# Optimization experiments

Measured on AMD Instinct MI355X. Metric: run time of the kernel, lower is better.

## Reference

```python
import jax, jax.numpy as jnp
import numpy as np

B, N, F, IMF = 16, 64, 512, 2048
EPS = 1e-5


def _linear_params(key, out_f, in_f):
    k1, k2 = jax.random.split(key)
    w = jax.random.normal(k1, (out_f, in_f), dtype=jnp.float32) * 0.02
    b = jax.random.normal(k2, (out_f,), dtype=jnp.float32) * 0.02
    return w, b


def setup_inputs() -> dict:
    key = jax.random.key(0)
    ks = jax.random.split(key, 8)
    inp = {}
    inp["input"] = jax.random.normal(ks[0], (B, N, F), dtype=jnp.float32)
    inp["im_input"] = jax.random.normal(ks[1], (B, IMF), dtype=jnp.float32)
    inp["gmlp1_w"], inp["gmlp1_b"] = _linear_params(ks[2], F, 2 * F)
    inp["gmlp2_w"], inp["gmlp2_b"] = _linear_params(ks[3], F, F)
    inp["gmlp3_w"], inp["gmlp3_b"] = _linear_params(ks[4], F, F)
    inp["im_w"], inp["im_b"] = _linear_params(ks[5], F, IMF)
    inp["bn_gamma"] = jnp.ones((F,), dtype=jnp.float32)
    inp["bn_beta"] = jnp.zeros((F,), dtype=jnp.float32)
    inp["d1_w"], inp["d1_b"] = _linear_params(ks[6], F, 2 * F)
    inp["d2_w"], inp["d2_b"] = _linear_params(ks[7], 2, F)
    return inp


def reference(input, im_input, gmlp1_w, gmlp1_b, gmlp2_w, gmlp2_b,
              gmlp3_w, gmlp3_b, im_w, im_b, bn_gamma, bn_beta,
              d1_w, d1_b, d2_w, d2_b):
    b, n, f = input.shape
    npair = n * n
    # relation_embedding: all-pairs expand + concat (replicating the exact
    # row-major reshape semantics of the original torch code, including the
    # memory-reinterpreting view used for feature2)
    feature1 = jnp.broadcast_to(input[:, None, :, :], (b, n, n, f)).reshape(b, npair, f)
    feature2 = jnp.broadcast_to(input[:, :, :, None], (b, n, f, n)).reshape(b, npair, f)
    feature = jnp.concatenate([feature1, feature2], axis=2).reshape(-1, 2 * f)  # [b*n^2, 1024]
    h = jax.nn.relu(feature @ gmlp1_w.T + gmlp1_b)
    h = jax.nn.relu(h @ gmlp2_w.T + gmlp2_b)
    h = jax.nn.relu(h @ gmlp3_w.T + gmlp3_b)
    sent_embedding = h.reshape(b, npair, f).mean(axis=1)  # [b, 512]
    # im_embedding: Linear + BatchNorm1d (training-mode batch stats) + ReLU
    img = im_input @ im_w.T + im_b
    mu = img.mean(axis=0)
    var = jnp.mean(jnp.square(img - mu), axis=0)  # biased variance
    img = bn_gamma * (img - mu) * jax.lax.rsqrt(var + EPS) + bn_beta
    img_embedding = jax.nn.relu(img)
    # net_D
    emb = jnp.concatenate([sent_embedding, img_embedding], axis=1)  # [b, 1024]
    out = jax.nn.relu(emb @ d1_w.T + d1_b) @ d2_w.T + d2_b  # [b, 2]
    return out
```

## Files before the change

kernel.cpp:

```cpp
#include <hip/hip_runtime.h>


typedef float f32x4 __attribute__((ext_vector_type(4)));
typedef __bf16 bf16x8v __attribute__((ext_vector_type(8)));
typedef __bf16 bf16x4v __attribute__((ext_vector_type(4)));

#define WS_A1Q     0u
#define WS_W1P     2097152u
#define WS_SENT    2129920u
#define WS_Y       2162688u
#define WS_IMGEMB  2195456u
#define WS_W2BF    2228224u
#define WS_W3BF    2752512u

__global__ __launch_bounds__(256) void k_prep(
    const float* __restrict__ input, const float* __restrict__ im_input,
    const float* __restrict__ g1w, const float* __restrict__ g1b,
    const float* __restrict__ g2w, const float* __restrict__ g3w,
    const float* __restrict__ imw, const float* __restrict__ imb,
    float* __restrict__ ws)
{
  __shared__ float As[16][72];
  __shared__ float Bs[16][72];
  const int blk = blockIdx.x, t = threadIdx.x;
  float4* A1Q = (float4*)ws;
  __bf16* w1p = (__bf16*)((char*)ws + WS_W1P);
  float* sent = (float*)((char*)ws + WS_SENT);
  float* yv   = (float*)((char*)ws + WS_Y);
  __bf16* w2bf = (__bf16*)((char*)ws + WS_W2BF);
  __bf16* w3bf = (__bf16*)((char*)ws + WS_W3BF);

  if (blk < 128) {
    const int tm = blk >> 3, tn = blk & 7;
    const int m0 = tm * 64, o0 = tn * 64;
    const int ty = t >> 4, tx = t & 15;
    const int lrow = t >> 2, lk4 = (t & 3) * 4;
    float acc[4][4] = {};
    for (int kc = 0; kc < 512; kc += 16) {
      float4 av = *(const float4*)(input + (m0 + lrow) * 512 + kc + lk4);
      float4 bw = *(const float4*)(g1w + (size_t)(o0 + lrow) * 1024 + kc + lk4);
      __syncthreads();
      As[lk4 + 0][lrow] = av.x; As[lk4 + 1][lrow] = av.y;
      As[lk4 + 2][lrow] = av.z; As[lk4 + 3][lrow] = av.w;
      Bs[lk4 + 0][lrow] = bw.x; Bs[lk4 + 1][lrow] = bw.y;
      Bs[lk4 + 2][lrow] = bw.z; Bs[lk4 + 3][lrow] = bw.w;
      __syncthreads();
#pragma unroll
      for (int kk = 0; kk < 16; ++kk) {
        float a4[4], b4[4];
        *(float4*)a4 = *(const float4*)&As[kk][4 * ty];
        *(float4*)b4 = *(const float4*)&Bs[kk][4 * tx];
#pragma unroll
        for (int ii = 0; ii < 4; ++ii)
#pragma unroll
          for (int jj = 0; jj < 4; ++jj)
            acc[ii][jj] += a4[ii] * b4[jj];
      }
    }
    float4 bias = *(const float4*)(g1b + o0 + 4 * tx);
#pragma unroll
    for (int ii = 0; ii < 4; ++ii) {
      float4 v;
      v.x = acc[ii][0] + bias.x; v.y = acc[ii][1] + bias.y;
      v.z = acc[ii][2] + bias.z; v.w = acc[ii][3] + bias.w;
      A1Q[(tm * 128 + tn * 16 + tx) * 64 + 4 * ty + ii] = v;
    }
  } else if (blk < 384) {
    int idx = ((blk - 128) * 256 + t) * 8;
    const float* src; __bf16* dst; int off;
    if (idx < 262144) { src = g2w; dst = w2bf; off = idx; }
    else              { src = g3w; dst = w3bf; off = idx - 262144; }
    int o = off >> 9, k = off & 511;
    int ks = k >> 5, quad = (k >> 3) & 3;
    int doff = (o >> 4) * 8192 + ks * 512 + (quad * 16 + (o & 15)) * 8;
    float4 v0 = *(const float4*)(src + off);
    float4 v1 = *(const float4*)(src + off + 4);
    bf16x8v h;
    h[0] = (__bf16)v0.x; h[1] = (__bf16)v0.y; h[2] = (__bf16)v0.z; h[3] = (__bf16)v0.w;
    h[4] = (__bf16)v1.x; h[5] = (__bf16)v1.y; h[6] = (__bf16)v1.z; h[7] = (__bf16)v1.w;
    *(bf16x8v*)(dst + doff) = h;
  } else if (blk < 400) {
    int idx = (blk - 384) * 256 + t;
    int o = idx >> 3, s = idx & 7;
    const float* p = g1w + (size_t)o * 1024 + 512 + s * 64;
    float sum = 0.f;
#pragma unroll
    for (int u = 0; u < 64; u += 4) {
      float4 v = *(const float4*)(p + u);
      sum += v.x + v.y + v.z + v.w;
    }
    int base = (o >> 4) * 512 + (o & 15) * 8 + s;
    w1p[base]       = (__bf16)sum;
    w1p[base + 128] = (__bf16)0.f;
    w1p[base + 256] = (__bf16)0.f;
    w1p[base + 384] = (__bf16)0.f;
    sent[idx] = 0.f; sent[idx + 4096] = 0.f;
  } else {
    int o = blk - 400;
    int wv = t >> 6, l = t & 63;
    const float* wrow = imw + (size_t)o * 2048;
    for (int bb = 0; bb < 4; ++bb) {
      int b = wv * 4 + bb;
      const float* xr = im_input + (size_t)b * 2048;
      float s = 0.f;
#pragma unroll
      for (int u = 0; u < 8; ++u) {
        int k = u * 256 + l * 4;
        float4 xv = *(const float4*)(xr + k);
        float4 wx = *(const float4*)(wrow + k);
        s += xv.x * wx.x + xv.y * wx.y + xv.z * wx.z + xv.w * wx.w;
      }
#pragma unroll
      for (int m = 32; m >= 1; m >>= 1) s += __shfl_xor(s, m);
      if (l == 0) yv[b * 512 + o] = s + imb[o];
    }
  }
}

__device__ __forceinline__ void kloop(const __bf16* __restrict__ wl,
                                      const __bf16* __restrict__ hbuf,
                                      int p16, int quad, f32x4 acc[4][8])
{
  const int msk3 = (p16 & 7) << 3;
  int moff[8];
#pragma unroll
  for (int mt = 0; mt < 8; ++mt)
    moff[mt] = (mt >> 2) * 32768 + (p16 + 16 * (mt & 3)) * 512;
  bf16x8v a[4], an[4];
#pragma unroll
  for (int ot = 0; ot < 4; ++ot) a[ot] = *(const bf16x8v*)(wl + ot * 8192);
#pragma unroll 2
  for (int ks = 0; ks < 16; ++ks) {
    const int kcb = (((ks * 4 + quad) << 3) ^ msk3);
    bf16x8v bf[8];
#pragma unroll
    for (int mt = 0; mt < 8; ++mt)
      bf[mt] = *(const bf16x8v*)(hbuf + moff[mt] + kcb);
    if (ks < 15) {
#pragma unroll
      for (int ot = 0; ot < 4; ++ot)
        an[ot] = *(const bf16x8v*)(wl + (ks + 1) * 512 + ot * 8192);
    }
#pragma unroll
    for (int ot = 0; ot < 4; ++ot)
#pragma unroll
      for (int mt = 0; mt < 4; ++mt)
        acc[ot][mt] = __builtin_amdgcn_mfma_f32_16x16x32_bf16(a[ot], bf[mt], acc[ot][mt], 0, 0, 0);
#pragma unroll
    for (int ot = 0; ot < 4; ++ot)
#pragma unroll
      for (int mt = 4; mt < 8; ++mt)
        acc[ot][mt] = __builtin_amdgcn_mfma_f32_16x16x32_bf16(a[ot], bf[mt], acc[ot][mt], 0, 0, 0);
    if (ks < 15) {
#pragma unroll
      for (int ot = 0; ot < 4; ++ot) a[ot] = an[ot];
    }
  }
}

__global__ __launch_bounds__(512, 2) void k_main(
    const float* __restrict__ input,
    const float* __restrict__ g2b, const float* __restrict__ g3b,
    const float* __restrict__ bng, const float* __restrict__ bnb,
    float* __restrict__ ws)
{
  const int blk = blockIdx.x, t = threadIdx.x;
  const float4* A1Q = (const float4*)ws;
  const __bf16* w1p = (const __bf16*)((char*)ws + WS_W1P);
  float* sent = (float*)((char*)ws + WS_SENT);
  float* yv   = (float*)((char*)ws + WS_Y);
  float* imge = (float*)((char*)ws + WS_IMGEMB);
  const __bf16* w2bf = (const __bf16*)((char*)ws + WS_W2BF);
  const __bf16* w3bf = (const __bf16*)((char*)ws + WS_W3BF);

  if (blk == 512) {
    int o = t;
    float vals[16];
    float mu = 0.f;
#pragma unroll
    for (int b = 0; b < 16; ++b) { vals[b] = yv[b * 512 + o]; mu += vals[b]; }
    mu *= (1.f / 16.f);
    float var = 0.f;
#pragma unroll
    for (int b = 0; b < 16; ++b) { float d = vals[b] - mu; var += d * d; }
    var *= (1.f / 16.f);
    float sc = bng[o] * rsqrtf(var + 1e-5f);
    float sh = bnb[o] - mu * sc;
#pragma unroll
    for (int b = 0; b < 16; ++b)
      imge[b * 512 + o] = fmaxf(vals[b] * sc + sh, 0.f);
    return;
  }

  __shared__ __align__(16) __bf16 hbuf[65536];

  const int b = blk >> 5, ipair = blk & 31;
  const int w = t >> 6, l = t & 63;
  const int quad = l >> 4, p16 = l & 15;

  float xreg0[8], xreg1[8];
  {
    const float* xr0 = input + (size_t)(b * 64 + ipair * 2) * 512 + l * 8;
    *(float4*)xreg0       = *(const float4*)xr0;
    *(float4*)(xreg0 + 4) = *(const float4*)(xr0 + 4);
    *(float4*)xreg1       = *(const float4*)(xr0 + 512);
    *(float4*)(xreg1 + 4) = *(const float4*)(xr0 + 516);
  }

  f32x4 acc[4][8];

  {
    bf16x8v xb[8];
#pragma unroll
    for (int mt = 0; mt < 4; ++mt) {
#pragma unroll
      for (int j = 0; j < 8; ++j) {
        float v0 = __shfl(xreg0[j], p16 + 16 * mt);
        float v1 = __shfl(xreg1[j], p16 + 16 * mt);
        xb[mt][j]     = (quad == 0) ? (__bf16)v0 : (__bf16)0.f;
        xb[mt + 4][j] = (quad == 0) ? (__bf16)v1 : (__bf16)0.f;
      }
    }
#pragma unroll
    for (int ot = 0; ot < 4; ++ot)
#pragma unroll
      for (int mt = 0; mt < 8; ++mt) { f32x4 z = {0.f, 0.f, 0.f, 0.f}; acc[ot][mt] = z; }
#pragma unroll
    for (int ot = 0; ot < 4; ++ot) {
      bf16x8v af = *(const bf16x8v*)(w1p + (w * 4 + ot) * 512 + l * 8);
#pragma unroll
      for (int mt = 0; mt < 8; ++mt)
        acc[ot][mt] = __builtin_amdgcn_mfma_f32_16x16x32_bf16(af, xb[mt], acc[ot][mt], 0, 0, 0);
    }
    const float4* cq = A1Q + ((size_t)b * 128 + w * 16) * 64;
#pragma unroll
    for (int ot = 0; ot < 4; ++ot) {
#pragma unroll
      for (int mtp = 0; mtp < 4; ++mtp) {
        float4 c = cq[(ot * 4 + quad) * 64 + 16 * mtp + p16];
        int row = p16 + 16 * mtp;
        int col = w * 64 + ot * 16 + quad * 4;
        int addr = row * 512 + (((col >> 3) ^ (row & 7)) << 3) + (col & 7);
#pragma unroll
        for (int tau = 0; tau < 2; ++tau) {
          f32x4 v = acc[ot][tau * 4 + mtp];
          bf16x4v h;
          h[0] = (__bf16)fmaxf(v[0] + c.x, 0.f);
          h[1] = (__bf16)fmaxf(v[1] + c.y, 0.f);
          h[2] = (__bf16)fmaxf(v[2] + c.z, 0.f);
          h[3] = (__bf16)fmaxf(v[3] + c.w, 0.f);
          *(bf16x4v*)(hbuf + tau * 32768 + addr) = h;
        }
      }
    }
  }
  __syncthreads();

#pragma unroll
  for (int ot = 0; ot < 4; ++ot)
#pragma unroll
    for (int mt = 0; mt < 8; ++mt) { f32x4 z = {0.f, 0.f, 0.f, 0.f}; acc[ot][mt] = z; }

  kloop(w2bf + (size_t)(w * 4) * 8192 + l * 8, hbuf, p16, quad, acc);
  __syncthreads();
#pragma unroll
  for (int ot = 0; ot < 4; ++ot) {
    float4 b2 = *(const float4*)(g2b + w * 64 + ot * 16 + quad * 4);
#pragma unroll
    for (int mt = 0; mt < 8; ++mt) {
      f32x4 v = acc[ot][mt];
      bf16x4v h;
      h[0] = (__bf16)fmaxf(v[0] + b2.x, 0.f);
      h[1] = (__bf16)fmaxf(v[1] + b2.y, 0.f);
      h[2] = (__bf16)fmaxf(v[2] + b2.z, 0.f);
      h[3] = (__bf16)fmaxf(v[3] + b2.w, 0.f);
      int row = p16 + 16 * (mt & 3);
      int col = w * 64 + ot * 16 + quad * 4;
      *(bf16x4v*)(hbuf + (mt >> 2) * 32768 + row * 512 +
                  (((col >> 3) ^ (row & 7)) << 3) + (col & 7)) = h;
    }
  }
  __syncthreads();

#pragma unroll
  for (int ot = 0; ot < 4; ++ot)
#pragma unroll
    for (int mt = 0; mt < 8; ++mt) { f32x4 z = {0.f, 0.f, 0.f, 0.f}; acc[ot][mt] = z; }

  kloop(w3bf + (size_t)(w * 4) * 8192 + l * 8, hbuf, p16, quad, acc);

#pragma unroll
  for (int ot = 0; ot < 4; ++ot) {
    float4 b3 = *(const float4*)(g3b + w * 64 + ot * 16 + quad * 4);
    float bb[4] = {b3.x, b3.y, b3.z, b3.w};
#pragma unroll
    for (int r = 0; r < 4; ++r) {
      float s = 0.f;
#pragma unroll
      for (int mt = 0; mt < 8; ++mt) s += fmaxf(acc[ot][mt][r] + bb[r], 0.f);
      s += __shfl_xor(s, 1);
      s += __shfl_xor(s, 2);
      s += __shfl_xor(s, 4);
      s += __shfl_xor(s, 8);
      if (p16 == 0)
        atomicAdd(&sent[b * 512 + w * 64 + ot * 16 + quad * 4 + r], s * (1.0f / 4096.0f));
    }
  }
}

__global__ __launch_bounds__(128) void k_head(
    const float* __restrict__ d1w, const float* __restrict__ d1b,
    const float* __restrict__ d2w, const float* __restrict__ d2b,
    const float* __restrict__ ws, float* __restrict__ out)
{
  __shared__ float emb[1024];
  const float* sent = (const float*)((const char*)ws + WS_SENT);
  const float* imge = (const float*)((const char*)ws + WS_IMGEMB);
  const int b = blockIdx.x >> 2, sl = blockIdx.x & 3, t = threadIdx.x;
  ((float4*)emb)[t]       = ((const float4*)(sent + b * 512))[t];
  ((float4*)(emb + 512))[t] = ((const float4*)(imge + b * 512))[t];
  __syncthreads();
  const int w2 = t >> 6, l = t & 63;
  float p0 = 0.f, p1 = 0.f;
  for (int rr = 0; rr < 64; ++rr) {
    int row = sl * 128 + w2 * 64 + rr;
    const float* wr = d1w + (size_t)row * 1024 + l * 4;
    float s = 0.f;
#pragma unroll
    for (int c = 0; c < 4; ++c) {
      float4 wv = *(const float4*)(wr + c * 256);
      float4 ev = *(const float4*)(emb + l * 4 + c * 256);
      s += wv.x * ev.x + wv.y * ev.y + wv.z * ev.z + wv.w * ev.w;
    }
#pragma unroll
    for (int m = 32; m >= 1; m >>= 1) s += __shfl_xor(s, m);
    float h = fmaxf(s + d1b[row], 0.f);
    p0 += d2w[row] * h;
    p1 += d2w[512 + row] * h;
  }
  if (l == 0) {
    if (sl == 0 && w2 == 0) { p0 += d2b[0]; p1 += d2b[1]; }
    atomicAdd(&out[b * 2 + 0], p0);
    atomicAdd(&out[b * 2 + 1], p1);
  }
}

extern "C" void kernel_launch(void* const* d_in, const int* in_sizes, int n_in,
                              void* d_out, int out_size, void* d_ws, size_t ws_size,
                              hipStream_t stream)
{
  const float* input    = (const float*)d_in[0];
  const float* im_input = (const float*)d_in[1];
  const float* g1w = (const float*)d_in[2];
  const float* g1b = (const float*)d_in[3];
  const float* g2w = (const float*)d_in[4];
  const float* g2b = (const float*)d_in[5];
  const float* g3w = (const float*)d_in[6];
  const float* g3b = (const float*)d_in[7];
  const float* imw = (const float*)d_in[8];
  const float* imb = (const float*)d_in[9];
  const float* bng = (const float*)d_in[10];
  const float* bnb = (const float*)d_in[11];
  const float* d1w = (const float*)d_in[12];
  const float* d1b = (const float*)d_in[13];
  const float* d2w = (const float*)d_in[14];
  const float* d2b = (const float*)d_in[15];
  float* out = (float*)d_out;
  float* ws  = (float*)d_ws;

  hipMemsetAsync(d_out, 0, (size_t)out_size * 4, stream);
  k_prep<<<912, 256, 0, stream>>>(input, im_input, g1w, g1b, g2w, g3w, imw, imb, ws);
  k_main<<<513, 512, 0, stream>>>(input, g2b, g3b, bng, bnb, ws);
  k_head<<<64, 128, 0, stream>>>(d1w, d1b, d2w, d2b, ws, out);
}
```

Before: 201.0 us.

## Move first-layer projection GEMM to bf16 MFMA kernel and drop memset/atomics in head

Replaces the FP32 LDS-tiled GEMM for the first half of gmlp1 (input × W1a) with a separate kernel that first converts W1a to a swizzled bf16 layout, then runs bf16 MFMA over each batch's 64 rows held in LDS. The weight-conversion blocks absorb W1a alongside W2/W3. The head kernel now uses one 512-thread block per batch with a shared-memory reduction instead of atomics, which removes the output memset. This adds one kernel launch and lowers the precision of the A1 projection to bf16. The new kernel launches only 16 blocks, so it uses few CUs.

Result: faster. 194.9 us (-3.0%).

```diff
diff --git a/kernel.cpp b/kernel.cpp
--- a/kernel.cpp
+++ b/kernel.cpp
@@ -12,69 +12,36 @@
 #define WS_IMGEMB  2195456u
 #define WS_W2BF    2228224u
 #define WS_W3BF    2752512u
-
-__global__ __launch_bounds__(256) void k_prep(
-    const float* __restrict__ input, const float* __restrict__ im_input,
-    const float* __restrict__ g1w, const float* __restrict__ g1b,
+#define WS_W1ABF   3276800u
+
+__global__ __launch_bounds__(256) void k_conv(
+    const float* __restrict__ im_input, const float* __restrict__ g1w,
     const float* __restrict__ g2w, const float* __restrict__ g3w,
     const float* __restrict__ imw, const float* __restrict__ imb,
     float* __restrict__ ws)
 {
-  __shared__ float As[16][72];
-  __shared__ float Bs[16][72];
   const int blk = blockIdx.x, t = threadIdx.x;
-  float4* A1Q = (float4*)ws;
-  __bf16* w1p = (__bf16*)((char*)ws + WS_W1P);
-  float* sent = (float*)((char*)ws + WS_SENT);
-  float* yv   = (float*)((char*)ws + WS_Y);
+  __bf16* w1p  = (__bf16*)((char*)ws + WS_W1P);
+  float* sent  = (float*)((char*)ws + WS_SENT);
+  float* yv    = (float*)((char*)ws + WS_Y);
+  __bf16* w1abf = (__bf16*)((char*)ws + WS_W1ABF);
   __bf16* w2bf = (__bf16*)((char*)ws + WS_W2BF);
   __bf16* w3bf = (__bf16*)((char*)ws + WS_W3BF);
 
-  if (blk < 128) {
-    const int tm = blk >> 3, tn = blk & 7;
-    const int m0 = tm * 64, o0 = tn * 64;
-    const int ty = t >> 4, tx = t & 15;
-    const int lrow = t >> 2, lk4 = (t & 3) * 4;
-    float acc[4][4] = {};
-    for (int kc = 0; kc < 512; kc += 16) {
-      float4 av = *(const float4*)(input + (m0 + lrow) * 512 + kc + lk4);
-      float4 bw = *(const float4*)(g1w + (size_t)(o0 + lrow) * 1024 + kc + lk4);
-      __syncthreads();
-      As[lk4 + 0][lrow] = av.x; As[lk4 + 1][lrow] = av.y;
-      As[lk4 + 2][lrow] = av.z; As[lk4 + 3][lrow] = av.w;
-      Bs[lk4 + 0][lrow] = bw.x; Bs[lk4 + 1][lrow] = bw.y;
-      Bs[lk4 + 2][lrow] = bw.z; Bs[lk4 + 3][lrow] = bw.w;
-      __syncthreads();
-#pragma unroll
-      for (int kk = 0; kk < 16; ++kk) {
-        float a4[4], b4[4];
-        *(float4*)a4 = *(const float4*)&As[kk][4 * ty];
-        *(float4*)b4 = *(const float4*)&Bs[kk][4 * tx];
-#pragma unroll
-        for (int ii = 0; ii < 4; ++ii)
-#pragma unroll
-          for (int jj = 0; jj < 4; ++jj)
-            acc[ii][jj] += a4[ii] * b4[jj];
-      }
-    }
-    float4 bias = *(const float4*)(g1b + o0 + 4 * tx);
-#pragma unroll
-    for (int ii = 0; ii < 4; ++ii) {
-      float4 v;
-      v.x = acc[ii][0] + bias.x; v.y = acc[ii][1] + bias.y;
-      v.z = acc[ii][2] + bias.z; v.w = acc[ii][3] + bias.w;
-      A1Q[(tm * 128 + tn * 16 + tx) * 64 + 4 * ty + ii] = v;
-    }
-  } else if (blk < 384) {
-    int idx = ((blk - 128) * 256 + t) * 8;
-    const float* src; __bf16* dst; int off;
-    if (idx < 262144) { src = g2w; dst = w2bf; off = idx; }
-    else              { src = g3w; dst = w3bf; off = idx - 262144; }
+  if (blk < 384) {
+    int idx = (blk * 256 + t) * 8;
+    int mat = idx >> 18;
+    int off = idx & 262143;
     int o = off >> 9, k = off & 511;
+    const float* src;
+    __bf16* dst;
+    if (mat == 0)      { src = g1w + (size_t)o * 1024 + k; dst = w1abf; }
+    else if (mat == 1) { src = g2w + off; dst = w2bf; }
+    else               { src = g3w + off; dst = w3bf; }
     int ks = k >> 5, quad = (k >> 3) & 3;
     int doff = (o >> 4) * 8192 + ks * 512 + (quad * 16 + (o & 15)) * 8;
-    float4 v0 = *(const float4*)(src + off);
-    float4 v1 = *(const float4*)(src + off + 4);
+    float4 v0 = *(const float4*)src;
+    float4 v1 = *(const float4*)(src + 4);
     bf16x8v h;
     h[0] = (__bf16)v0.x; h[1] = (__bf16)v0.y; h[2] = (__bf16)v0.z; h[3] = (__bf16)v0.w;
     h[4] = (__bf16)v1.x; h[5] = (__bf16)v1.y; h[6] = (__bf16)v1.z; h[7] = (__bf16)v1.w;
@@ -117,6 +84,86 @@
   }
 }
 
+__device__ __forceinline__ void kloop4(const __bf16* __restrict__ wl,
+                                       const __bf16* __restrict__ hb,
+                                       int p16, int quad, f32x4 acc[4][4])
+{
+  const int msk3 = (p16 & 7) << 3;
+  bf16x8v a[4], an[4];
+#pragma unroll
+  for (int ot = 0; ot < 4; ++ot) a[ot] = *(const bf16x8v*)(wl + ot * 8192);
+#pragma unroll 2
+  for (int ks = 0; ks < 16; ++ks) {
+    const int kcb = (((ks * 4 + quad) << 3) ^ msk3);
+    bf16x8v bf[4];
+#pragma unroll
+    for (int mt = 0; mt < 4; ++mt)
+      bf[mt] = *(const bf16x8v*)(hb + (p16 + 16 * mt) * 512 + kcb);
+    if (ks < 15) {
+#pragma unroll
+      for (int ot = 0; ot < 4; ++ot)
+        an[ot] = *(const bf16x8v*)(wl + (ks + 1) * 512 + ot * 8192);
+    }
+#pragma unroll
+    for (int ot = 0; ot < 4; ++ot)
+#pragma unroll
+      for (int mt = 0; mt < 4; ++mt)
+        acc[ot][mt] = __builtin_amdgcn_mfma_f32_16x16x32_bf16(a[ot], bf[mt], acc[ot][mt], 0, 0, 0);
+    if (ks < 15) {
+#pragma unroll
+      for (int ot = 0; ot < 4; ++ot) a[ot] = an[ot];
+    }
+  }
+}
+
+__global__ __launch_bounds__(512) void k_prepA1(
+    const float* __restrict__ input, const float* __restrict__ g1b,
+    float* __restrict__ ws)
+{
+  __shared__ __align__(16) __bf16 xbuf[32768];
+  const int b = blockIdx.x, t = threadIdx.x;
+  const __bf16* w1abf = (const __bf16*)((char*)ws + WS_W1ABF);
+  float* A1Qf = (float*)ws;
+
+#pragma unroll
+  for (int q = 0; q < 8; ++q) {
+    int id = t + 512 * q;
+    int r = id >> 6, oc = id & 63;
+    const float* src = input + (size_t)(b * 64 + r) * 512 + oc * 8;
+    float4 v0 = *(const float4*)src;
+    float4 v1 = *(const float4*)(src + 4);
+    bf16x8v h;
+    h[0] = (__bf16)v0.x; h[1] = (__bf16)v0.y; h[2] = (__bf16)v0.z; h[3] = (__bf16)v0.w;
+    h[4] = (__bf16)v1.x; h[5] = (__bf16)v1.y; h[6] = (__bf16)v1.z; h[7] = (__bf16)v1.w;
+    *(bf16x8v*)(xbuf + r * 512 + ((oc ^ (r & 7)) << 3)) = h;
+  }
+  __syncthreads();
+
+  const int w = t >> 6, l = t & 63;
+  const int quad = l >> 4, p16 = l & 15;
+  f32x4 acc[4][4];
+#pragma unroll
+  for (int ot = 0; ot < 4; ++ot)
+#pragma unroll
+    for (int mt = 0; mt < 4; ++mt) { f32x4 z = {0.f, 0.f, 0.f, 0.f}; acc[ot][mt] = z; }
+
+  kloop4(w1abf + (size_t)(w * 4) * 8192 + l * 8, xbuf, p16, quad, acc);
+
+#pragma unroll
+  for (int ot = 0; ot < 4; ++ot) {
+    float4 bias = *(const float4*)(g1b + w * 64 + ot * 16 + quad * 4);
+    float bb[4] = {bias.x, bias.y, bias.z, bias.w};
+#pragma unroll
+    for (int mt = 0; mt < 4; ++mt) {
+#pragma unroll
+      for (int r = 0; r < 4; ++r) {
+        size_t o4 = (size_t)b * 128 + w * 16 + ot * 4 + quad;
+        A1Qf[(o4 * 64 + mt * 16 + p16) * 4 + r] = acc[ot][mt][r] + bb[r];
+      }
+    }
+  }
+}
+
 __device__ __forceinline__ void kloop(const __bf16* __restrict__ wl,
                                       const __bf16* __restrict__ hbuf,
                                       int p16, int quad, f32x4 acc[4][8])
@@ -308,22 +355,23 @@
   }
 }
 
-__global__ __launch_bounds__(128) void k_head(
+__global__ __launch_bounds__(512) void k_head(
     const float* __restrict__ d1w, const float* __restrict__ d1b,
     const float* __restrict__ d2w, const float* __restrict__ d2b,
     const float* __restrict__ ws, float* __restrict__ out)
 {
   __shared__ float emb[1024];
+  __shared__ float red[8][2];
   const float* sent = (const float*)((const char*)ws + WS_SENT);
   const float* imge = (const float*)((const char*)ws + WS_IMGEMB);
-  const int b = blockIdx.x >> 2, sl = blockIdx.x & 3, t = threadIdx.x;
-  ((float4*)emb)[t]       = ((const float4*)(sent + b * 512))[t];
-  ((float4*)(emb + 512))[t] = ((const float4*)(imge + b * 512))[t];
-  __syncthreads();
-  const int w2 = t >> 6, l = t & 63;
+  const int b = blockIdx.x, t = threadIdx.x;
+  emb[t]       = sent[b * 512 + t];
+  emb[512 + t] = imge[b * 512 + t];
+  __syncthreads();
+  const int v = t >> 6, l = t & 63;
   float p0 = 0.f, p1 = 0.f;
   for (int rr = 0; rr < 64; ++rr) {
-    int row = sl * 128 + w2 * 64 + rr;
+    int row = v * 64 + rr;
     const float* wr = d1w + (size_t)row * 1024 + l * 4;
     float s = 0.f;
 #pragma unroll
@@ -338,10 +386,14 @@
     p0 += d2w[row] * h;
     p1 += d2w[512 + row] * h;
   }
-  if (l == 0) {
-    if (sl == 0 && w2 == 0) { p0 += d2b[0]; p1 += d2b[1]; }
-    atomicAdd(&out[b * 2 + 0], p0);
-    atomicAdd(&out[b * 2 + 1], p1);
+  if (l == 0) { red[v][0] = p0; red[v][1] = p1; }
+  __syncthreads();
+  if (t == 0) {
+    float q0 = d2b[0], q1 = d2b[1];
+#pragma unroll
+    for (int u = 0; u < 8; ++u) { q0 += red[u][0]; q1 += red[u][1]; }
+    out[b * 2 + 0] = q0;
+    out[b * 2 + 1] = q1;
   }
 }
 
@@ -368,8 +420,8 @@
   float* out = (float*)d_out;
   float* ws  = (float*)d_ws;
 
-  hipMemsetAsync(d_out, 0, (size_t)out_size * 4, stream);
-  k_prep<<<912, 256, 0, stream>>>(input, im_input, g1w, g1b, g2w, g3w, imw, imb, ws);
+  k_conv<<<912, 256, 0, stream>>>(im_input, g1w, g2w, g3w, imw, imb, ws);
+  k_prepA1<<<16, 512, 0, stream>>>(input, g1b, ws);
   k_main<<<513, 512, 0, stream>>>(input, g2b, g3b, bng, bnb, ws);
-  k_head<<<64, 128, 0, stream>>>(d1w, d1b, d2w, d2b, ws, out);
-}
+  k_head<<<16, 512, 0, stream>>>(d1w, d1b, d2w, d2b, ws, out);
+}
```
